# Optimization experiments

Measured on AMD Instinct MI355X. Metric: run time of the kernel, lower is better.

## Reference

```python
import jax, jax.numpy as jnp
import numpy as np
import math

B, T, D = 2, 2048, 2048
H, DH = 16, 128
DKV, DQ, DR = 512, 1024, 64
ROPE_BASE = 500000.0
EPS = 1e-6
SCALE = 1.0 / math.sqrt(DH + DR)


def setup_inputs() -> dict:
    key = jax.random.key(0)
    ks = jax.random.split(key, 12)
    s = 0.02
    return {
        'x': jax.random.normal(ks[0], (B, T, D), jnp.float32),
        'W_DQ': jax.random.normal(ks[1], (D, DQ), jnp.float32) * s,
        'W_UQ': jax.random.normal(ks[2], (DQ, H * DH), jnp.float32) * s,
        'W_QR': jax.random.normal(ks[3], (DQ, H * DR), jnp.float32) * s,
        'W_DKV': jax.random.normal(ks[4], (D, DKV), jnp.float32) * s,
        'W_UK': jax.random.normal(ks[5], (DKV, H * DH), jnp.float32) * s,
        'W_UV': jax.random.normal(ks[6], (DKV, H * DH), jnp.float32) * s,
        'W_KR': jax.random.normal(ks[7], (D, DR), jnp.float32) * s,
        'W_O': jax.random.normal(ks[8], (H * DH, D), jnp.float32) * s,
        'q_norm_w': jnp.ones((DQ,), jnp.float32),
        'kv_norm_w': jnp.ones((DKV,), jnp.float32),
    }


def _rmsnorm(v, w):
    n = jax.lax.rsqrt(jnp.mean(v * v, axis=-1, keepdims=True) + EPS)
    return v * n * w


def _rotate_half(v):
    v1, v2 = jnp.split(v, 2, axis=-1)
    return jnp.concatenate([-v2, v1], axis=-1)


def _rope_tables(seq_len):
    inv_freq = 1.0 / (ROPE_BASE ** (jnp.arange(0, DR, 2, dtype=jnp.float32) / DR))
    t = jnp.arange(seq_len, dtype=jnp.float32)
    freqs = jnp.outer(t, inv_freq)              # (S, DR/2)
    emb = jnp.concatenate([freqs, freqs], -1)   # (S, DR)
    return jnp.cos(emb), jnp.sin(emb)


def reference(x, W_DQ, W_UQ, W_QR, W_DKV, W_UK, W_UV, W_KR, W_O, q_norm_w, kv_norm_w):
    # Query path: low-rank compress -> RMSNorm -> up-project (content + rope parts)
    c_Q = _rmsnorm(x @ W_DQ, q_norm_w)                               # (B,T,DQ)
    q_C = (c_Q @ W_UQ).reshape(B, T, H, DH).transpose(0, 2, 1, 3)    # (B,H,T,DH)
    q_R = (c_Q @ W_QR).reshape(B, T, H, DR).transpose(0, 2, 1, 3)    # (B,H,T,DR)
    # KV path: joint low-rank latent + decoupled rope key
    c_KV = _rmsnorm(x @ W_DKV, kv_norm_w)                            # (B,T,DKV)
    k_C = (c_KV @ W_UK).reshape(B, T, H, DH).transpose(0, 2, 1, 3)   # (B,H,T,DH)
    v_C = (c_KV @ W_UV).reshape(B, T, H, DH).transpose(0, 2, 1, 3)   # (B,H,T,DH)
    k_R = (x @ W_KR)[:, None, :, :]                                  # (B,1,T,DR) shared across heads
    # Decoupled RoPE
    cos, sin = _rope_tables(T)
    cos = cos[None, None]; sin = sin[None, None]                     # (1,1,T,DR)
    q_R = q_R * cos + _rotate_half(q_R) * sin
    k_R = k_R * cos + _rotate_half(k_R) * sin
    k_R = jnp.broadcast_to(k_R, (B, H, T, DR))
    q = jnp.concatenate([q_C, q_R], axis=-1)                         # (B,H,T,DH+DR)
    k = jnp.concatenate([k_C, k_R], axis=-1)
    # Causal attention with MLA scale 1/sqrt(d_head + d_rope)
    scores = jnp.einsum('bhqd,bhkd->bhqk', q, k) * SCALE
    causal = jnp.tril(jnp.ones((T, T), bool))
    scores = jnp.where(causal, scores, jnp.finfo(scores.dtype).min)
    attn = jax.nn.softmax(scores, axis=-1)
    out = jnp.einsum('bhqk,bhkd->bhqd', attn, v_C)                   # (B,H,T,DH)
    out = out.transpose(0, 2, 1, 3).reshape(B, T, H * DH)
    return out @ W_O                                                 # (B,T,D)
```

## Files before the change

### kernel.cpp

```cpp
#include <hip/hip_runtime.h>
#include <cstdint>
#include <cstddef>

#define B_   2
#define T_   2048
#define D_   2048
#define H_   16
#define DH_  128
#define DQ_  1024
#define DKV_ 512
#define DR_  64
#define M_   4096
#define SCALE_ 0.07216878364870323f
#define SC2_   0.10412808709930322f
#define LN_BASE_ 13.122363377404328f

typedef unsigned short u16;
typedef __attribute__((ext_vector_type(8))) short short8;
typedef __attribute__((ext_vector_type(4))) float f32x4;

__device__ __forceinline__ float b2f(u16 u) { return __uint_as_float(((uint32_t)u) << 16); }
__device__ __forceinline__ u16 f2b(float f) {
    uint32_t x = __float_as_uint(f);
    return (u16)((x + 0x7fffu + ((x >> 16) & 1u)) >> 16);
}
__device__ __forceinline__ u16 f2b_fast(float f) {
    return (u16)((__float_as_uint(f) + 0x8000u) >> 16);
}

__device__ __forceinline__ void gload_lds16(const u16* src, u16* dst) {
    __builtin_amdgcn_global_load_lds(
        (const __attribute__((address_space(1))) uint32_t*)(uintptr_t)src,
        (__attribute__((address_space(3))) uint32_t*)(uintptr_t)dst, 16, 0, 0);
}

struct TPack {
    const float* src[8];
    u16*         dst[8];
    int K[8];
    int N[8];
    int ntx[8];
    int start[9];
};

__global__ __launch_bounds__(256) void prep_k(TPack p, const float* __restrict__ x,
                                              u16* __restrict__ xb, int ntr) {
    const int bid = blockIdx.x;
    if (bid < ntr) {
        __shared__ float tile[32][33];
        int w = 0;
#pragma unroll
        for (int i = 1; i < 8; ++i) if (bid >= p.start[i]) w = i;
        const int lt = bid - p.start[w];
        const int bx = lt % p.ntx[w], by = lt / p.ntx[w];
        const float* in = p.src[w];
        u16* out = p.dst[w];
        const int K = p.K[w], N = p.N[w];
        const int k0 = by * 32, n0 = bx * 32;
        const int tx = threadIdx.x & 31, ty = threadIdx.x >> 5;
#pragma unroll
        for (int i = 0; i < 4; ++i) {
            int k = k0 + ty + i * 8;
            int n = n0 + tx;
            tile[ty + i * 8][tx] = (n < N) ? in[(size_t)k * N + n] : 0.f;
        }
        __syncthreads();
#pragma unroll
        for (int i = 0; i < 4; ++i) {
            int n = n0 + ty + i * 8;
            out[(size_t)n * K + k0 + tx] = f2b(tile[tx][ty + i * 8]);
        }
    } else {
        const int i = ((bid - ntr) * 256 + threadIdx.x) * 4;
        const float4 v = *(const float4*)(x + i);
        ushort4 o;
        o.x = f2b(v.x); o.y = f2b(v.y); o.z = f2b(v.z); o.w = f2b(v.w);
        *(ushort4*)(xb + i) = o;
    }
}

template <int OUT_BF16>
__global__ __launch_bounds__(256) void gemm_tn(const u16* __restrict__ A,
                                               const u16* __restrict__ Bt,
                                               void* __restrict__ Cv,
                                               int N, int K) {
    __shared__ __attribute__((aligned(16))) u16 lA[128 * 32];
    __shared__ __attribute__((aligned(16))) u16 lB[128 * 32];
    const int m0 = blockIdx.y * 128, n0 = blockIdx.x * 128;
    const int tid = threadIdx.x, wave = tid >> 6, lane = tid & 63;
    const int wm = (wave >> 1) * 64, wn = (wave & 1) * 64;
    const int r = lane & 15, kq = lane >> 4;

    f32x4 acc[4][4];
#pragma unroll
    for (int i = 0; i < 4; ++i)
#pragma unroll
        for (int j = 0; j < 4; ++j) acc[i][j] = (f32x4){0.f, 0.f, 0.f, 0.f};

    for (int kk = 0; kk < K; kk += 32) {
#pragma unroll
        for (int p = 0; p < 2; ++p) {
            const int c = p * 256 + wave * 64 + lane;
            const u16* ga = A  + (size_t)(m0 + (c >> 2)) * K + kk + (c & 3) * 8;
            const u16* gb = Bt + (size_t)(n0 + (c >> 2)) * K + kk + (c & 3) * 8;
            u16* la = lA + (size_t)(p * 256 + wave * 64) * 8;
            u16* lb = lB + (size_t)(p * 256 + wave * 64) * 8;
            gload_lds16(ga, la);
            gload_lds16(gb, lb);
        }
        __syncthreads();
        short8 av[4], bv[4];
#pragma unroll
        for (int mi = 0; mi < 4; ++mi)
            av[mi] = *(const short8*)&lA[(wm + mi * 16 + r) * 32 + kq * 8];
#pragma unroll
        for (int ni = 0; ni < 4; ++ni)
            bv[ni] = *(const short8*)&lB[(wn + ni * 16 + r) * 32 + kq * 8];
#pragma unroll
        for (int mi = 0; mi < 4; ++mi)
#pragma unroll
            for (int ni = 0; ni < 4; ++ni)
                acc[mi][ni] = __builtin_amdgcn_mfma_f32_16x16x32_bf16(
                    av[mi], bv[ni], acc[mi][ni], 0, 0, 0);
        __syncthreads();
    }
    const int r4 = (lane >> 4) * 4, cc = lane & 15;
#pragma unroll
    for (int mi = 0; mi < 4; ++mi)
#pragma unroll
        for (int ni = 0; ni < 4; ++ni)
#pragma unroll
            for (int i = 0; i < 4; ++i) {
                const int row = m0 + wm + mi * 16 + r4 + i;
                const int col = n0 + wn + ni * 16 + cc;
                const float v = acc[mi][ni][i];
                if (OUT_BF16) ((u16*)Cv)[(size_t)row * N + col] = f2b(v);
                else          ((float*)Cv)[(size_t)row * N + col] = v;
            }
}

#define S_BM 256
#define S_BN 256
#define S_BK 64

__device__ __forceinline__ void gemm256_core(
    const u16* __restrict__ A, const u16* __restrict__ Bt, int K,
    int m0, int n0, int tid, f32x4 (&acc)[8][4],
    u16 (*sA)[S_BM * S_BK], u16 (*sB)[S_BN * S_BK]) {
    const int lane = tid & 63;
    const int wave = tid >> 6;
    const int wm = wave >> 2;
    const int r = lane & 15, kq = lane >> 4;
    const int wn = wave & 3;

    const u16* gA[4]; const u16* gB[4]; int dOf[4];
#pragma unroll
    for (int is = 0; is < 4; ++is) {
        const int c = is * 512 + tid;
        const int row = c >> 3, c16 = c & 7;
        gA[is] = A  + (size_t)(m0 + row) * K + ((c16 ^ (row & 7)) * 8);
        gB[is] = Bt + (size_t)(n0 + row) * K + ((c16 ^ (row & 7)) * 8);
        dOf[is] = c * 8;
    }

    const int NKT = K >> 6;

    auto STG = [&](int arr, int half, int bs, int kk) {
        u16* dst = arr ? (u16*)sB[bs] : (u16*)sA[bs];
        const u16** g = arr ? gB : gA;
#pragma unroll
        for (int is = half * 2; is < half * 2 + 2; ++is)
            gload_lds16(g[is] + kk, dst + dOf[is]);
    };

    STG(0, 0, 0, 0); STG(0, 1, 0, 0); STG(1, 0, 0, 0); STG(1, 1, 0, 0);

    short8 af[4][2], bf[2][2];
    for (int kt = 0; kt < NKT; ++kt) {
        const int cur = kt & 1;
        const int kk = (kt + 1) * 64;
        const int pf = (kt + 1 < NKT);
        const u16* cA = sA[cur];
        const u16* cB = sB[cur];

        auto lda = [&](int row, int g) -> short8 {
            return *(const short8*)&cA[row * 64 + ((g ^ (row & 7)) * 8)];
        };
        auto ldb = [&](int row, int g) -> short8 {
            return *(const short8*)&cB[row * 64 + ((g ^ (row & 7)) * 8)];
        };

#pragma unroll
        for (int ph = 0; ph < 4; ++ph) {
            const int mh = ph >> 1;
            const int nh = (ph == 1 || ph == 2) ? 1 : 0;
            if (pf) STG(ph >> 1, ph & 1, cur ^ 1, kk);
            if (ph == 0) {
                if (pf) asm volatile("s_waitcnt vmcnt(2)" ::: "memory");
                else    asm volatile("s_waitcnt vmcnt(0)" ::: "memory");
            }
            __builtin_amdgcn_s_barrier();
            asm volatile("" ::: "memory");
            if (!(ph & 1)) {
#pragma unroll
                for (int mi = 0; mi < 4; ++mi)
#pragma unroll
                    for (int ks = 0; ks < 2; ++ks)
                        af[mi][ks] = lda(wm * 128 + mh * 64 + mi * 16 + r, ks * 4 + kq);
            }
#pragma unroll
            for (int ni = 0; ni < 2; ++ni)
#pragma unroll
                for (int ks = 0; ks < 2; ++ks)
                    bf[ni][ks] = ldb(wn * 64 + nh * 32 + ni * 16 + r, ks * 4 + kq);
#pragma unroll
            for (int ks = 0; ks < 2; ++ks)
#pragma unroll
                for (int mi = 0; mi < 4; ++mi)
#pragma unroll
                    for (int ni = 0; ni < 2; ++ni)
                        acc[mh * 4 + mi][nh * 2 + ni] =
                            __builtin_amdgcn_mfma_f32_16x16x32_bf16(
                                af[mi][ks], bf[ni][ks],
                                acc[mh * 4 + mi][nh * 2 + ni], 0, 0, 0);
            asm volatile("" ::: "memory");
            __builtin_amdgcn_s_barrier();
            asm volatile("" ::: "memory");
        }
    }
}

__global__ __launch_bounds__(512, 1) void gemm256p_k(
    const u16* __restrict__ A0, const u16* __restrict__ B0,
    u16* __restrict__ C0, int N0c, int K0,
    const u16* __restrict__ A1, const u16* __restrict__ B1,
    u16* __restrict__ C1, int N1c, int K1,
    u16* __restrict__ Vt, int vcol0, int nx0)
{
    __shared__ __attribute__((aligned(16))) u16 sA[2][S_BM * S_BK];
    __shared__ __attribute__((aligned(16))) u16 sB[2][S_BN * S_BK];
    const int sel = (int)blockIdx.x >= nx0;
    const u16* A  = sel ? A1 : A0;
    const u16* Bt = sel ? B1 : B0;
    const int  K  = sel ? K1 : K0;
    const int lbx = sel ? (blockIdx.x - nx0) : blockIdx.x;
    const int m0 = blockIdx.y * S_BM, n0 = lbx * S_BN;
    const int tid = threadIdx.x, lane = tid & 63;
    const int wave = tid >> 6, wm = wave >> 2, wn = wave & 3;
    const int kq = lane >> 4;

    f32x4 acc[8][4];
#pragma unroll
    for (int i = 0; i < 8; ++i)
#pragma unroll
        for (int j = 0; j < 4; ++j) acc[i][j] = (f32x4){0.f, 0.f, 0.f, 0.f};

    gemm256_core(A, Bt, K, m0, n0, tid, acc, sA, sB);

    const int r4c = kq * 4, cc = lane & 15;
    if (!sel) {
#pragma unroll
        for (int mf = 0; mf < 8; ++mf)
#pragma unroll
            for (int nf = 0; nf < 4; ++nf)
#pragma unroll
                for (int i = 0; i < 4; ++i) {
                    const int row = m0 + wm * 128 + mf * 16 + r4c + i;
                    const int col = n0 + wn * 64 + nf * 16 + cc;
                    C0[(size_t)row * N0c + col] = f2b(acc[mf][nf][i]);
                }
    } else if (n0 < vcol0) {
#pragma unroll
        for (int mf = 0; mf < 8; ++mf)
#pragma unroll
            for (int nf = 0; nf < 4; ++nf)
#pragma unroll
                for (int i = 0; i < 4; ++i) {
                    const int row = m0 + wm * 128 + mf * 16 + r4c + i;
                    const int col = n0 + wn * 64 + nf * 16 + cc;
                    C1[(size_t)row * N1c + col] = f2b(acc[mf][nf][i]);
                }
    } else {
#pragma unroll
        for (int mf = 0; mf < 8; ++mf)
#pragma unroll
            for (int nf = 0; nf < 4; ++nf) {
                const int tp = m0 + wm * 128 + mf * 16 + r4c;
                const int c  = n0 - vcol0 + wn * 64 + nf * 16 + cc;
                u16 tmp[4];
#pragma unroll
                for (int i = 0; i < 4; ++i) tmp[i] = f2b(acc[mf][nf][i]);
                *(ushort4*)&Vt[((size_t)((tp >> 11) * 2048 + c)) * 2048 + (tp & 2047)]
                    = *(ushort4*)tmp;
            }
    }
}

__global__ __launch_bounds__(512, 1) void gemm256o_k(
    const u16* __restrict__ A, const u16* __restrict__ Bt,
    float* __restrict__ Cf, int N, int K)
{
    __shared__ __attribute__((aligned(16))) u16 sA[2][S_BM * S_BK];
    __shared__ __attribute__((aligned(16))) u16 sB[2][S_BN * S_BK];
    const int m0 = blockIdx.y * S_BM, n0 = blockIdx.x * S_BN;
    const int tid = threadIdx.x, lane = tid & 63;
    const int wave = tid >> 6, wm = wave >> 2, wn = wave & 3;
    const int kq = lane >> 4;

    f32x4 acc[8][4];
#pragma unroll
    for (int i = 0; i < 8; ++i)
#pragma unroll
        for (int j = 0; j < 4; ++j) acc[i][j] = (f32x4){0.f, 0.f, 0.f, 0.f};

    gemm256_core(A, Bt, K, m0, n0, tid, acc, sA, sB);

    const int r4c = kq * 4, cc = lane & 15;
#pragma unroll
    for (int mf = 0; mf < 8; ++mf)
#pragma unroll
        for (int nf = 0; nf < 4; ++nf)
#pragma unroll
            for (int i = 0; i < 4; ++i) {
                const int row = m0 + wm * 128 + mf * 16 + r4c + i;
                const int col = n0 + wn * 64 + nf * 16 + cc;
                Cf[(size_t)row * N + col] = acc[mf][nf][i];
            }
}

__global__ __launch_bounds__(256) void normrope_k(const u16* __restrict__ P1,
                                                  const float* __restrict__ qnw,
                                                  const float* __restrict__ kvnw,
                                                  u16* __restrict__ cQb,
                                                  u16* __restrict__ cKVb,
                                                  u16* __restrict__ kRb) {
    const int which = blockIdx.y;
    if (which < 2) {
        const int row = blockIdx.x;
        const int N = which ? 512 : 1024;
        const int off = which ? 1024 : 0;
        const float* w = which ? kvnw : qnw;
        u16* outp = which ? cKVb : cQb;
        const u16* src = P1 + (size_t)row * 1664 + off;
        const int j = threadIdx.x * 4;
        float v[4] = {0.f, 0.f, 0.f, 0.f};
        if (j < N) {
            ushort4 u = *(const ushort4*)(src + j);
            v[0] = b2f(u.x); v[1] = b2f(u.y); v[2] = b2f(u.z); v[3] = b2f(u.w);
        }
        float ss = v[0]*v[0] + v[1]*v[1] + v[2]*v[2] + v[3]*v[3];
#pragma unroll
        for (int offc = 32; offc; offc >>= 1) ss += __shfl_down(ss, offc);
        __shared__ float red[4];
        const int wave = threadIdx.x >> 6, lane = threadIdx.x & 63;
        if (lane == 0) red[wave] = ss;
        __syncthreads();
        const float tot = red[0] + red[1] + red[2] + red[3];
        const float sc = rsqrtf(tot / (float)N + 1e-6f);
        if (j < N) {
            ushort4 o;
            o.x = f2b(v[0] * sc * w[j]);
            o.y = f2b(v[1] * sc * w[j + 1]);
            o.z = f2b(v[2] * sc * w[j + 2]);
            o.w = f2b(v[3] * sc * w[j + 3]);
            *(ushort4*)(outp + (size_t)row * N + j) = o;
        }
    } else {
        if (blockIdx.x >= 1024) return;
        const int row = blockIdx.x * 4 + (threadIdx.x >> 6);
        const int j = threadIdx.x & 63;
        const int t = row & (T_ - 1);
        const int i = j & 31;
        const float invf = __expf(-LN_BASE_ * (float)(2 * i) * (1.0f / 64.0f));
        const float ang = (float)t * invf;
        const float c = cosf(ang), s = sinf(ang);
        const u16* src = P1 + (size_t)row * 1664 + 1536;
        const float v = b2f(src[j]);
        const float rot = (j < 32) ? -b2f(src[j + 32]) : b2f(src[j - 32]);
        kRb[(size_t)row * 64 + j] = f2b(v * c + rot * s);
    }
}

#define ABQ  128
#define ABK  64
#define NW   8
#define KSTR 200
#define VSTR 72
#define PSTR 72
#define VOFF 12800
#define KVSZ 22016
#define QSTRIDE 3072
#define KSTRIDE 4096

__global__ __launch_bounds__(512, 1) void attn_mfma_k(
    const u16* __restrict__ qC,
    const u16* __restrict__ kC, const u16* __restrict__ kR,
    const u16* __restrict__ Vt, u16* __restrict__ outp)
{
    __shared__ __attribute__((aligned(16))) u16 sKV[3][KVSZ];
    __shared__ __attribute__((aligned(16))) u16 sP[NW * 16 * PSTR];

    const int h = blockIdx.x, b = blockIdx.z;
    const int qb = b ? (15 - (int)blockIdx.y) : (int)blockIdx.y;
    const int q0 = qb * ABQ;
    const int tid = threadIdx.x, wave = tid >> 6, lane = tid & 63;
    const int r = lane & 15, kq = lane >> 4, r4 = kq * 4;
    const int wq = wave * 16;

    const u16* gsrc[6]; int gstep[6]; int doff[6];
#pragma unroll
    for (int j = 0; j < 6; ++j) {
        const int i = wave + NW * j;
        const int slot = (i < 43) ? i : (i - 43);
        if (slot < 25) {
            const int s = slot * 64 + lane;
            const int rr2 = s / 25;
            int cc = s - rr2 * 25;
            if (cc > 23) cc = 0;
            if (cc < 16) {
                gsrc[j] = kC + (size_t)(b * T_ + rr2) * KSTRIDE + h * 128 + cc * 8;
                gstep[j] = ABK * KSTRIDE;
            } else {
                gsrc[j] = kR + (size_t)(b * T_ + rr2) * 64 + (cc - 16) * 8;
                gstep[j] = ABK * 64;
            }
            doff[j] = slot * 512;
        } else {
            const int sl = slot - 25;
            const int s = sl * 64 + lane;
            const int rr2 = s / 9;
            int cc = s - rr2 * 9;
            if (cc > 7) cc = 0;
            gsrc[j] = Vt + ((size_t)(b * H_ + h) * 128 + rr2) * T_ + cc * 8;
            gstep[j] = ABK;
            doff[j] = VOFF + sl * 512;
        }
    }

    short8 qf[6];
    {
        const int t = q0 + wq + r;
        const u16* qcrow = qC + (size_t)(b * T_ + t) * QSTRIDE + h * 128 + kq * 8;
#pragma unroll
        for (int kc = 0; kc < 4; ++kc) qf[kc] = *(const short8*)(qcrow + kc * 32);
        const u16* qrraw = qC + (size_t)(b * T_ + t) * QSTRIDE + 2048 + h * 64 + kq * 8;
        const short8 q0v = *(const short8*)(qrraw);
        const short8 q1v = *(const short8*)(qrraw + 32);
        short8 o0, o1;
#pragma unroll
        for (int j = 0; j < 8; ++j) {
            const int i = kq * 8 + j;
            const float invf = __expf(-LN_BASE_ * (float)(2 * i) * (1.0f / 64.0f));
            const float ang = (float)t * invf;
            const float cs = cosf(ang), sn = sinf(ang);
            const float a = b2f((u16)q0v[j]), bb = b2f((u16)q1v[j]);
            o0[j] = (short)f2b(a * cs - bb * sn);
            o1[j] = (short)f2b(bb * cs + a * sn);
        }
        qf[4] = o0; qf[5] = o1;
    }

    f32x4 Oa[8];
#pragma unroll
    for (int nt = 0; nt < 8; ++nt) Oa[nt] = (f32x4){0.f, 0.f, 0.f, 0.f};
    float Lrow[4] = {0.f, 0.f, 0.f, 0.f};

    u16* myP = sP + wave * 16 * PSTR;

    auto STAGE = [&](int kt2, int bs) {
        u16* dst = &sKV[bs][0];
#pragma unroll
        for (int j = 0; j < 6; ++j)
            gload_lds16(gsrc[j] + (size_t)kt2 * (size_t)gstep[j], dst + doff[j]);
    };

    const int nkt = 2 * qb + 2;
    STAGE(0, 0);
    STAGE(1, 1);
    for (int kt = 0; kt < nkt; ++kt) {
        const int cur = kt % 3;
        if (kt == 0 || kt >= nkt - 1) {
            asm volatile("s_waitcnt vmcnt(0)" ::: "memory");
        } else {
            asm volatile("s_waitcnt vmcnt(6)" ::: "memory");
        }
        __builtin_amdgcn_s_barrier();
        asm volatile("" ::: "memory");

        const u16* cK = &sKV[cur][0];
        const u16* cV = &sKV[cur][VOFF];
        const int k0 = kt * ABK;

        f32x4 Sa[4];
#pragma unroll
        for (int nt = 0; nt < 4; ++nt) Sa[nt] = (f32x4){0.f, 0.f, 0.f, 0.f};
#pragma unroll
        for (int kc = 0; kc < 6; ++kc) {
            short8 kf[4];
#pragma unroll
            for (int nt = 0; nt < 4; ++nt)
                kf[nt] = *(const short8*)&cK[(nt * 16 + r) * KSTR + (kc * 4 + kq) * 8];
#pragma unroll
            for (int nt = 0; nt < 4; ++nt)
                Sa[nt] = __builtin_amdgcn_mfma_f32_16x16x32_bf16(
                    qf[kc], kf[nt], Sa[nt], 0, 0, 0);
        }

        if (kt < nkt - 2) {
#pragma unroll
            for (int i = 0; i < 4; ++i) {
                float sm = 0.f;
#pragma unroll
                for (int nt = 0; nt < 4; ++nt) {
                    const float p = exp2f(Sa[nt][i] * SC2_);
                    sm += p;
                    myP[(r4 + i) * PSTR + nt * 16 + r] = f2b_fast(p);
                }
                Lrow[i] += sm;
            }
        } else {
#pragma unroll
            for (int i = 0; i < 4; ++i) {
                const int grow = q0 + wq + r4 + i;
                float sm = 0.f;
#pragma unroll
                for (int nt = 0; nt < 4; ++nt) {
                    float p = exp2f(Sa[nt][i] * SC2_);
                    p = (k0 + nt * 16 + r > grow) ? 0.f : p;
                    sm += p;
                    myP[(r4 + i) * PSTR + nt * 16 + r] = f2b_fast(p);
                }
                Lrow[i] += sm;
            }
        }

#pragma unroll
        for (int kc2 = 0; kc2 < 2; ++kc2) {
            const short8 pf = *(const short8*)&myP[r * PSTR + (kc2 * 4 + kq) * 8];
#pragma unroll
            for (int nt = 0; nt < 8; ++nt) {
                const short8 vf = *(const short8*)&cV[(nt * 16 + r) * VSTR + (kc2 * 4 + kq) * 8];
                Oa[nt] = __builtin_amdgcn_mfma_f32_16x16x32_bf16(
                    pf, vf, Oa[nt], 0, 0, 0);
            }
        }

        if (kt + 2 < nkt) STAGE(kt + 2, (kt + 2) % 3);
    }

#pragma unroll
    for (int i = 0; i < 4; ++i) {
        float L = Lrow[i];
        L += __shfl_xor(L, 1);
        L += __shfl_xor(L, 2);
        L += __shfl_xor(L, 4);
        L += __shfl_xor(L, 8);
        const float inv = 1.0f / L;
        const int t = q0 + wq + r4 + i;
        u16* orow = outp + (size_t)(b * T_ + t) * 2048 + h * 128;
#pragma unroll
        for (int nt = 0; nt < 8; ++nt)
            orow[nt * 16 + r] = f2b(Oa[nt][i] * inv);
    }
}

extern "C" void kernel_launch(void* const* d_in, const int* in_sizes, int n_in,
                              void* d_out, int out_size, void* d_ws, size_t ws_size,
                              hipStream_t stream) {
    (void)in_sizes; (void)n_in; (void)out_size; (void)ws_size;
    const float* x     = (const float*)d_in[0];
    const float* W_DQ  = (const float*)d_in[1];
    const float* W_UQ  = (const float*)d_in[2];
    const float* W_QR  = (const float*)d_in[3];
    const float* W_DKV = (const float*)d_in[4];
    const float* W_UK  = (const float*)d_in[5];
    const float* W_UV  = (const float*)d_in[6];
    const float* W_KR  = (const float*)d_in[7];
    const float* W_O   = (const float*)d_in[8];
    const float* qnw   = (const float*)d_in[9];
    const float* kvnw  = (const float*)d_in[10];
    float* out = (float*)d_out;

    char* base = (char*)d_ws;
    size_t o = 0;
    auto alloc = [&](size_t bytes) {
        char* r = base + o;
        o += (bytes + 255) & ~(size_t)255;
        return r;
    };
    u16* WT1  = (u16*)alloc((size_t)1664 * 2048 * 2);
    u16* WT2  = (u16*)alloc((size_t)3072 * 1024 * 2);
    u16* WT3  = (u16*)alloc((size_t)4096 * 512 * 2);
    u16* WT_O = (u16*)alloc((size_t)2048 * 2048 * 2);
    u16* xb   = (u16*)alloc((size_t)M_ * 2048 * 2);
    u16* U1   = (u16*)alloc((size_t)M_ * 2048 * 2);
    u16* P2   = (u16*)alloc((size_t)M_ * 3072 * 2);
    u16* P3   = (u16*)alloc((size_t)M_ * 4096 * 2);
    u16* cQb  = (u16*)alloc((size_t)M_ * 1024 * 2);
    u16* cKVb = (u16*)alloc((size_t)M_ * 512 * 2);
    u16* qRb  = (u16*)alloc((size_t)M_ * 1024 * 2);
    u16* kRb  = (u16*)alloc((size_t)M_ * 64 * 2);
    (void)qRb;
    u16* P1       = U1;
    u16* attn_out = U1;
    u16* Vt       = xb;

    TPack tp;
    const float* srcs[8] = {W_DQ, W_DKV, W_KR, W_UQ, W_QR, W_UK, W_UV, W_O};
    u16* dsts[8] = {WT1, WT1 + (size_t)1024*2048, WT1 + (size_t)1536*2048,
                    WT2, WT2 + (size_t)2048*1024,
                    WT3, WT3 + (size_t)2048*512, WT_O};
    const int Ks[8]   = {2048, 2048, 2048, 1024, 1024, 512, 512, 2048};
    const int Ns[8]   = {1024,  512,   64, 2048, 1024, 2048, 2048, 2048};
    const int ntxs[8] = {  32,   16,    4,   64,   32,   64,   64,   64};
    int cum = 0;
    for (int i = 0; i < 8; ++i) {
        tp.src[i] = srcs[i]; tp.dst[i] = dsts[i];
        tp.K[i] = Ks[i]; tp.N[i] = Ns[i]; tp.ntx[i] = ntxs[i];
        tp.start[i] = cum;
        cum += ntxs[i] * (Ks[i] / 32);
    }
    tp.start[8] = cum;
    const int ncast = (M_ * D_) / 1024;
    prep_k<<<cum + ncast, 256, 0, stream>>>(tp, x, xb, cum);

    gemm_tn<1><<<dim3(1664/128, M_/128), 256, 0, stream>>>(xb, WT1, (void*)P1, 1664, 2048);

    normrope_k<<<dim3(M_, 3), 256, 0, stream>>>(P1, qnw, kvnw, cQb, cKVb, kRb);

    gemm256p_k<<<dim3(3072/256 + 4096/256, M_/256), 512, 0, stream>>>(
        cQb,  WT2, P2, 3072, 1024,
        cKVb, WT3, P3, 4096, 512,
        Vt, 2048, 3072/256);

    attn_mfma_k<<<dim3(H_, T_/ABQ, B_), 512, 0, stream>>>(P2, P3, kRb, Vt, attn_out);

    gemm256o_k<<<dim3(2048/256, M_/256), 512, 0, stream>>>(attn_out, WT_O, out, 2048, 2048);
}
```

Baseline: 391.5 us.

## Swizzle attention LDS layout with XOR and use 128-tile GEMM for output projection

```diff
diff --git a/kernel.cpp b/kernel.cpp
--- a/kernel.cpp
+++ b/kernel.cpp
@@ -294,38 +294,6 @@
                     = *(ushort4*)tmp;
             }
     }
-}
-
-__global__ __launch_bounds__(512, 1) void gemm256o_k(
-    const u16* __restrict__ A, const u16* __restrict__ Bt,
-    float* __restrict__ Cf, int N, int K)
-{
-    __shared__ __attribute__((aligned(16))) u16 sA[2][S_BM * S_BK];
-    __shared__ __attribute__((aligned(16))) u16 sB[2][S_BN * S_BK];
-    const int m0 = blockIdx.y * S_BM, n0 = blockIdx.x * S_BN;
-    const int tid = threadIdx.x, lane = tid & 63;
-    const int wave = tid >> 6, wm = wave >> 2, wn = wave & 3;
-    const int kq = lane >> 4;
-
-    f32x4 acc[8][4];
-#pragma unroll
-    for (int i = 0; i < 8; ++i)
-#pragma unroll
-        for (int j = 0; j < 4; ++j) acc[i][j] = (f32x4){0.f, 0.f, 0.f, 0.f};
-
-    gemm256_core(A, Bt, K, m0, n0, tid, acc, sA, sB);
-
-    const int r4c = kq * 4, cc = lane & 15;
-#pragma unroll
-    for (int mf = 0; mf < 8; ++mf)
-#pragma unroll
-        for (int nf = 0; nf < 4; ++nf)
-#pragma unroll
-            for (int i = 0; i < 4; ++i) {
-                const int row = m0 + wm * 128 + mf * 16 + r4c + i;
-                const int col = n0 + wn * 64 + nf * 16 + cc;
-                Cf[(size_t)row * N + col] = acc[mf][nf][i];
-            }
 }
 
 __global__ __launch_bounds__(256) void normrope_k(const u16* __restrict__ P1,
@@ -384,11 +352,11 @@
 #define ABQ  128
 #define ABK  64
 #define NW   8
-#define KSTR 200
-#define VSTR 72
-#define PSTR 72
-#define VOFF 12800
-#define KVSZ 22016
+#define KSTR 192
+#define VSTR 64
+#define PSTR 64
+#define VOFF 12288
+#define KVSZ 20480
 #define QSTRIDE 3072
 #define KSTRIDE 4096
 
@@ -407,33 +375,32 @@
     const int r = lane & 15, kq = lane >> 4, r4 = kq * 4;
     const int wq = wave * 16;
 
-    const u16* gsrc[6]; int gstep[6]; int doff[6];
-#pragma unroll
-    for (int j = 0; j < 6; ++j) {
+    const u16* gsrc[5]; int gstep[5]; int doff[5];
+#pragma unroll
+    for (int j = 0; j < 5; ++j) {
         const int i = wave + NW * j;
-        const int slot = (i < 43) ? i : (i - 43);
-        if (slot < 25) {
-            const int s = slot * 64 + lane;
-            const int rr2 = s / 25;
-            int cc = s - rr2 * 25;
-            if (cc > 23) cc = 0;
-            if (cc < 16) {
-                gsrc[j] = kC + (size_t)(b * T_ + rr2) * KSTRIDE + h * 128 + cc * 8;
+        if (i < 24) {
+            const int s = i * 64 + lane;
+            const int rr2 = s / 24;
+            const int cc = s - rr2 * 24;
+            const int scc = cc ^ (rr2 & 7);
+            if (scc < 16) {
+                gsrc[j] = kC + (size_t)(b * T_ + rr2) * KSTRIDE + h * 128 + scc * 8;
                 gstep[j] = ABK * KSTRIDE;
             } else {
-                gsrc[j] = kR + (size_t)(b * T_ + rr2) * 64 + (cc - 16) * 8;
+                gsrc[j] = kR + (size_t)(b * T_ + rr2) * 64 + (scc - 16) * 8;
                 gstep[j] = ABK * 64;
             }
-            doff[j] = slot * 512;
+            doff[j] = i * 512;
         } else {
-            const int sl = slot - 25;
-            const int s = sl * 64 + lane;
-            const int rr2 = s / 9;
-            int cc = s - rr2 * 9;
-            if (cc > 7) cc = 0;
-            gsrc[j] = Vt + ((size_t)(b * H_ + h) * 128 + rr2) * T_ + cc * 8;
+            const int iv = i - 24;
+            const int s = iv * 64 + lane;
+            const int rr2 = s >> 3;
+            const int cc = s & 7;
+            const int scc = cc ^ (rr2 & 7);
+            gsrc[j] = Vt + ((size_t)(b * H_ + h) * 128 + rr2) * T_ + scc * 8;
             gstep[j] = ABK;
-            doff[j] = VOFF + sl * 512;
+            doff[j] = VOFF + iv * 512;
         }
     }
 
@@ -465,12 +432,13 @@
     for (int nt = 0; nt < 8; ++nt) Oa[nt] = (f32x4){0.f, 0.f, 0.f, 0.f};
     float Lrow[4] = {0.f, 0.f, 0.f, 0.f};
 
-    u16* myP = sP + wave * 16 * PSTR;
+    u16* myP = sP + (size_t)wave * 16 * PSTR;
+    const int re = r & 7;
 
     auto STAGE = [&](int kt2, int bs) {
         u16* dst = &sKV[bs][0];
 #pragma unroll
-        for (int j = 0; j < 6; ++j)
+        for (int j = 0; j < 5; ++j)
             gload_lds16(gsrc[j] + (size_t)kt2 * (size_t)gstep[j], dst + doff[j]);
     };
 
@@ -482,7 +450,7 @@
         if (kt == 0 || kt >= nkt - 1) {
             asm volatile("s_waitcnt vmcnt(0)" ::: "memory");
         } else {
-            asm volatile("s_waitcnt vmcnt(6)" ::: "memory");
+            asm volatile("s_waitcnt vmcnt(5)" ::: "memory");
         }
         __builtin_amdgcn_s_barrier();
         asm volatile("" ::: "memory");
@@ -499,7 +467,8 @@
             short8 kf[4];
 #pragma unroll
             for (int nt = 0; nt < 4; ++nt)
-                kf[nt] = *(const short8*)&cK[(nt * 16 + r) * KSTR + (kc * 4 + kq) * 8];
+                kf[nt] = *(const short8*)&cK[(nt * 16 + r) * KSTR
+                                            + (((kc * 4 + kq) ^ re) * 8)];
 #pragma unroll
             for (int nt = 0; nt < 4; ++nt)
                 Sa[nt] = __builtin_amdgcn_mfma_f32_16x16x32_bf16(
@@ -509,26 +478,32 @@
         if (kt < nkt - 2) {
 #pragma unroll
             for (int i = 0; i < 4; ++i) {
+                const int prow = r4 + i;
+                const int pre = prow & 7;
                 float sm = 0.f;
 #pragma unroll
                 for (int nt = 0; nt < 4; ++nt) {
                     const float p = exp2f(Sa[nt][i] * SC2_);
                     sm += p;
-                    myP[(r4 + i) * PSTR + nt * 16 + r] = f2b_fast(p);
+                    myP[prow * PSTR + (((nt * 2 + (r >> 3)) ^ pre) * 8) + re]
+                        = f2b_fast(p);
                 }
                 Lrow[i] += sm;
             }
         } else {
 #pragma unroll
             for (int i = 0; i < 4; ++i) {
-                const int grow = q0 + wq + r4 + i;
+                const int prow = r4 + i;
+                const int pre = prow & 7;
+                const int grow = q0 + wq + prow;
                 float sm = 0.f;
 #pragma unroll
                 for (int nt = 0; nt < 4; ++nt) {
                     float p = exp2f(Sa[nt][i] * SC2_);
                     p = (k0 + nt * 16 + r > grow) ? 0.f : p;
                     sm += p;
-                    myP[(r4 + i) * PSTR + nt * 16 + r] = f2b_fast(p);
+                    myP[prow * PSTR + (((nt * 2 + (r >> 3)) ^ pre) * 8) + re]
+                        = f2b_fast(p);
                 }
                 Lrow[i] += sm;
             }
@@ -536,10 +511,12 @@
 
 #pragma unroll
         for (int kc2 = 0; kc2 < 2; ++kc2) {
-            const short8 pf = *(const short8*)&myP[r * PSTR + (kc2 * 4 + kq) * 8];
+            const short8 pf = *(const short8*)&myP[r * PSTR
+                                                  + (((kc2 * 4 + kq) ^ re) * 8)];
 #pragma unroll
             for (int nt = 0; nt < 8; ++nt) {
-                const short8 vf = *(const short8*)&cV[(nt * 16 + r) * VSTR + (kc2 * 4 + kq) * 8];
+                const short8 vf = *(const short8*)&cV[(nt * 16 + r) * VSTR
+                                                     + (((kc2 * 4 + kq) ^ re) * 8)];
                 Oa[nt] = __builtin_amdgcn_mfma_f32_16x16x32_bf16(
                     pf, vf, Oa[nt], 0, 0, 0);
             }
@@ -635,5 +612,5 @@
 
     attn_mfma_k<<<dim3(H_, T_/ABQ, B_), 512, 0, stream>>>(P2, P3, kRb, Vt, attn_out);
 
-    gemm256o_k<<<dim3(2048/256, M_/256), 512, 0, stream>>>(attn_out, WT_O, out, 2048, 2048);
-}
+    gemm_tn<0><<<dim3(2048/128, M_/128), 256, 0, stream>>>(attn_out, WT_O, (void*)out, 2048, 2048);
+}
```

Result: no change. 388.6 us (-0.7%).
